# Performance work log

Measured on AMD Instinct MI355X. Metric: run time of the kernel, lower is better.

The kernel has to match this reference:

```python
import jax, jax.numpy as jnp
import numpy as np

FULL_SCALE = 128.0
R = 0.5
TOPK = 4


def setup_inputs() -> dict:
    key = jax.random.key(0)
    k0, k1, k2, k3, k4 = jax.random.split(key, 5)
    B, Na, Nb, D = 16, 2048, 2048, 512
    coords_a = jax.random.randint(k0, (B, Na, 3), 0, 128, dtype=jnp.int32)
    coords_b = jax.random.randint(k1, (B, Nb, 3), 0, 128, dtype=jnp.int32)
    feats_a = jax.random.normal(k2, (B, Na, D), jnp.float32)
    feats_b = jax.random.normal(k3, (B, Nb, D), jnp.float32)
    W = jax.random.normal(k4, (2 * D, D), jnp.float32) / np.sqrt(2 * D).astype(np.float32)
    bias = jnp.zeros((D,), jnp.float32)
    return {"feats_a": feats_a, "feats_b": feats_b, "W": W, "bias": bias,
            "coords_a": coords_a, "coords_b": coords_b}


def _pairwise_l2(ca, cb):
    # ca: [B,Na,3], cb: [B,Nb,3] -> [B,Na,Nb], scaled by full_scale
    x2 = jnp.sum(ca * ca, axis=-1)[:, :, None]
    y2 = jnp.sum(cb * cb, axis=-1)[:, None, :]
    sq = x2 + y2 - 2.0 * jnp.einsum('bnd,bmd->bnm', ca, cb)
    return jnp.sqrt(jnp.clip(sq, 0.0, None)) / FULL_SCALE


def reference(feats_a, feats_b, W, bias, coords_a, coords_b):
    ca = coords_a.astype(jnp.float32)
    cb = coords_b.astype(jnp.float32)
    dist = _pairwise_l2(ca, cb)                       # [B,Na,Nb]
    neg_top, idx = jax.lax.top_k(-dist, TOPK)         # smallest TOPK distances
    dist_w = R - jnp.clip(-neg_top, 0.0, R)           # [B,Na,k]
    # gather neighbor features: [B,Na,k,D]
    b_f = jnp.take_along_axis(feats_b[:, None, :, :], idx[:, :, :, None], axis=2)
    a_f = feats_a[:, :, None, :]                      # broadcast over k
    h = jnp.concatenate([b_f, a_f - b_f], axis=-1)    # [B,Na,k,2D]
    fused = jnp.sum(jax.nn.relu(h @ W + bias) * dist_w[..., None], axis=2)  # [B,Na,D]
    # ME.cat(a, tmp): concatenate features along channel dim
    return jnp.concatenate([feats_a, fused], axis=-1)  # [B,Na,2D]
```

## Files before the change

### kernel.cpp

```cpp
#include <hip/hip_runtime.h>
#include <hip/hip_bf16.h>
#include <cstdint>
#include <cstddef>

#define NA   2048
#define NB   2048
#define DD   512
#define PADK 40

typedef __attribute__((ext_vector_type(8))) short bf16x8;
typedef __attribute__((ext_vector_type(4))) float f32x4;
typedef unsigned short u16;
typedef unsigned int   u32;

__device__ __forceinline__ u16 f2b_hw(float f) {
    u32 w;
    asm("v_cvt_pk_bf16_f32 %0, %1, %2" : "=v"(w) : "v"(f), "v"(f));
    return (u16)w;
}
__device__ __forceinline__ float b2f(u16 h) {
    return __uint_as_float(((u32)h) << 16);
}
__device__ __forceinline__ u32 umin32(u32 a, u32 b) { return a < b ? a : b; }
__device__ __forceinline__ u32 umax32(u32 a, u32 b) { return a > b ? a : b; }
__device__ __forceinline__ u32 med3u(u32 a, u32 b, u32 c) {
    return umax32(umin32(a, b), umin32(umax32(a, b), c));
}

#define GLDS16(gsrc, ldst)                                                  \
    __builtin_amdgcn_global_load_lds(                                       \
        (const __attribute__((address_space(1))) void*)(gsrc),              \
        (__attribute__((address_space(3))) void*)(ldst), 16, 0, 0)

__global__ __launch_bounds__(256) void prep_w(const float* __restrict__ W,
                                              u16* __restrict__ W2T,
                                              u16* __restrict__ WdT) {
    __shared__ float s2[64][65];
    __shared__ float sd[64][65];
    int kb = blockIdx.x * 64, nb = blockIdx.y * 64;
    int tid = threadIdx.x;
    int c = tid & 63, r0 = tid >> 6;
    #pragma unroll
    for (int p = 0; p < 16; ++p) {
        int r = p * 4 + r0;
        float w1 = W[(size_t)(kb + r) * DD + nb + c];
        float w2 = W[(size_t)(512 + kb + r) * DD + nb + c];
        s2[r][c] = w2;
        sd[r][c] = w1 - w2;
    }
    __syncthreads();
    #pragma unroll
    for (int p = 0; p < 16; ++p) {
        int n = p * 4 + r0;
        W2T[(size_t)(nb + n) * DD + kb + c] = f2b_hw(s2[c][n]);
        WdT[(size_t)(nb + n) * DD + kb + c] = f2b_hw(sd[c][n]);
    }
}

__global__ __launch_bounds__(512) void topk_kernel(const int* __restrict__ ca,
                                                   const int* __restrict__ cb,
                                                   int* __restrict__ idx_out,
                                                   float* __restrict__ w_out,
                                                   const float* __restrict__ fa,
                                                   float* __restrict__ out) {
    __shared__ u32 pcb[NB];
    __shared__ u32 part[3 * 128 * 4];
    int b = blockIdx.y;
    int tid = threadIdx.x;
    for (int p = tid; p < NB; p += 512) {
        const int* c = cb + ((size_t)b * NB + p) * 3;
        pcb[p] = (u32)c[0] | ((u32)c[1] << 8) | ((u32)c[2] << 16);
    }
    __syncthreads();

    int q = tid & 127, g = tid >> 7;
    int i = blockIdx.x * 128 + q;
    const int* ac = ca + ((size_t)b * NA + i) * 3;
    int ax = ac[0], ay = ac[1], az = ac[2];

    u32 k0 = ~0u, k1 = ~0u, k2 = ~0u, k3 = ~0u;
    int j0 = g * 512;
    #pragma unroll 8
    for (int jj = 0; jj < 512; ++jj) {
        int j = j0 + jj;
        u32 p = pcb[j];
        int dx = ax - (int)(p & 255u);
        int dy = ay - (int)((p >> 8) & 255u);
        int dz = az - (int)(p >> 16);
        u32 s = (u32)(__mul24(dx, dx) + __mul24(dy, dy) + __mul24(dz, dz));
        u32 key = (s << 11) | (u32)j;
        u32 nk0 = umin32(k0, key);
        u32 nk1 = med3u(key, k0, k1);
        u32 nk2 = med3u(key, k1, k2);
        u32 nk3 = med3u(key, k2, k3);
        k0 = nk0; k1 = nk1; k2 = nk2; k3 = nk3;
    }
    if (g) {
        u32* pp = &part[((g - 1) * 128 + q) * 4];
        pp[0] = k0; pp[1] = k1; pp[2] = k2; pp[3] = k3;
    }
    __syncthreads();
    if (g == 0) {
        #pragma unroll
        for (int L = 0; L < 3; ++L) {
            const u32* pp = &part[(L * 128 + q) * 4];
            #pragma unroll
            for (int t = 0; t < 4; ++t) {
                u32 key = pp[t];
                u32 nk0 = umin32(k0, key);
                u32 nk1 = med3u(key, k0, k1);
                u32 nk2 = med3u(key, k1, k2);
                u32 nk3 = med3u(key, k2, k3);
                k0 = nk0; k1 = nk1; k2 = nk2; k3 = nk3;
            }
        }
        size_t o = ((size_t)b * NA + i) * 4;
        u32 ks[4] = {k0, k1, k2, k3};
        #pragma unroll
        for (int t = 0; t < 4; ++t) {
            idx_out[o + t] = (int)(ks[t] & 2047u);
            float d = sqrtf((float)(ks[t] >> 11)) * (1.0f / 128.0f);
            w_out[o + t] = 0.5f - fminf(d, 0.5f);
        }
    }

    int cid = blockIdx.y * gridDim.x + blockIdx.x;
    const float* src = fa + (size_t)cid * 128 * DD;
    float* dst = out + (size_t)cid * 128 * 1024;
    #pragma unroll 4
    for (int it = 0; it < 32; ++it) {
        int flat = it * 512 + tid;
        int row = flat >> 7;
        int c4  = flat & 127;
        f32x4 v = *(const f32x4*)(src + (size_t)row * DD + c4 * 4);
        *(f32x4*)(dst + (size_t)row * 1024 + c4 * 4) = v;
    }
}

template<bool FUSED>
__global__ __launch_bounds__(256) void gemm_kernel(const float* __restrict__ A,
                                                   const u16* __restrict__ BT,
                                                   u16* __restrict__ C,
                                                   const int* __restrict__ idxb,
                                                   const float* __restrict__ wb,
                                                   const float* __restrict__ bias,
                                                   const u16* __restrict__ Qb,
                                                   float* __restrict__ out) {
    __shared__ __align__(16) char smem[FUSED ? 33792 : 26624];
    float* As = (float*)smem;
    u16*  Bs  = (u16*)(smem + 16384);

    const int tid  = threadIdx.x;
    const int lane = tid & 63;
    const int wave = tid >> 6;
    const int mb   = blockIdx.x;
    const int m0 = (((mb & 7) << 5) | (mb >> 3)) * 128;
    const int n0 = blockIdx.y * 128;
    const int l15 = lane & 15;
    const int lk8 = (lane >> 4) * 8;
    const int qa  = lk8 >> 2;

    const int srow  = lane >> 3;
    const int squad = (lane & 7) ^ srow;

    const int brow = tid >> 2;
    const int bcol = (tid & 3) * 8;

    const int wr = (wave >> 1) * 64;
    const int wc = (wave & 1) * 64;

    f32x4 acc[4][4];
    #pragma unroll
    for (int m = 0; m < 4; ++m)
        #pragma unroll
        for (int n = 0; n < 4; ++n)
            acc[m][n] = (f32x4){0.f, 0.f, 0.f, 0.f};

    int aoff[4][2];
    #pragma unroll
    for (int m = 0; m < 4; ++m) {
        int R = wr + m * 16 + l15;
        int sx = R & 7;
        aoff[m][0] = R * 128 + ((qa ^ sx) << 4);
        aoff[m][1] = R * 128 + (((qa + 1) ^ sx) << 4);
    }
    const char* AsB = (const char*)As;

    const float* asrc[4];
    #pragma unroll
    for (int p = 0; p < 4; ++p)
        asrc[p] = A + (size_t)(m0 + p * 32 + wave * 8 + srow) * DD + squad * 4;
    const u16* bsrc[2];
    #pragma unroll
    for (int p = 0; p < 2; ++p)
        bsrc[p] = BT + (size_t)(n0 + p * 64 + brow) * DD + bcol;

    for (int kk = 0; kk < DD; kk += 32) {
        bf16x8 bv0 = *(const bf16x8*)(bsrc[0] + kk);
        bf16x8 bv1 = *(const bf16x8*)(bsrc[1] + kk);
        #pragma unroll
        for (int p = 0; p < 4; ++p)
            GLDS16(asrc[p] + kk, As + (p * 32 + wave * 8) * 32);
        *(bf16x8*)(&Bs[brow * PADK + bcol]) = bv0;
        *(bf16x8*)(&Bs[(64 + brow) * PADK + bcol]) = bv1;
        __syncthreads();

        bf16x8 af[4], bfr[4];
        #pragma unroll
        for (int m = 0; m < 4; ++m) {
            f32x4 lo = *(const f32x4*)(AsB + aoff[m][0]);
            f32x4 hi = *(const f32x4*)(AsB + aoff[m][1]);
            u32 w0, w1, w2, w3;
            asm("v_cvt_pk_bf16_f32 %0, %1, %2" : "=v"(w0) : "v"(lo[0]), "v"(lo[1]));
            asm("v_cvt_pk_bf16_f32 %0, %1, %2" : "=v"(w1) : "v"(lo[2]), "v"(lo[3]));
            asm("v_cvt_pk_bf16_f32 %0, %1, %2" : "=v"(w2) : "v"(hi[0]), "v"(hi[1]));
            asm("v_cvt_pk_bf16_f32 %0, %1, %2" : "=v"(w3) : "v"(hi[2]), "v"(hi[3]));
            union { u32 u[4]; bf16x8 v; } cv;
            cv.u[0] = w0; cv.u[1] = w1; cv.u[2] = w2; cv.u[3] = w3;
            af[m] = cv.v;
        }
        #pragma unroll
        for (int n = 0; n < 4; ++n)
            bfr[n] = *(const bf16x8*)(&Bs[(wc + n * 16 + l15) * PADK + lk8]);

        #pragma unroll
        for (int m = 0; m < 4; ++m)
            #pragma unroll
            for (int n = 0; n < 4; ++n)
                acc[m][n] = __builtin_amdgcn_mfma_f32_16x16x32_bf16(
                    af[m], bfr[n], acc[m][n], 0, 0, 0);
        __syncthreads();
    }

    const int r4 = (lane >> 4) * 4;

    if (!FUSED) {
        #pragma unroll
        for (int m = 0; m < 4; ++m)
            #pragma unroll
            for (int n = 0; n < 4; ++n)
                #pragma unroll
                for (int j = 0; j < 4; ++j) {
                    int row = m0 + wr + m * 16 + r4 + j;
                    int col = n0 + wc + n * 16 + l15;
                    C[(size_t)row * DD + col] = f2b_hw(acc[m][n][j]);
                }
        return;
    }

    float bi[4];
    #pragma unroll
    for (int n = 0; n < 4; ++n)
        bi[n] = bias[n0 + wc + n * 16 + l15];

    u16* Ps = (u16*)smem;
    #pragma unroll
    for (int m = 0; m < 4; ++m)
        #pragma unroll
        for (int n = 0; n < 4; ++n)
            #pragma unroll
            for (int j = 0; j < 4; ++j)
                Ps[(wr + m * 16 + r4 + j) * 132 + (wc + n * 16 + l15)] =
                    f2b_hw(acc[m][n][j] + bi[n]);
    __syncthreads();

    const int g = tid >> 4, l16 = tid & 15;
    const int bb = m0 >> 11;
    const u16* qs = Qb + ((size_t)bb << 20);
    #pragma unroll
    for (int k = 0; k < 8; ++k) {
        const int r  = g * 8 + k;
        const int gr = m0 + r;
        int4  iv = *(const int4*)(idxb + (size_t)gr * 4);
        f32x4 wv = *(const f32x4*)(wb + (size_t)gr * 4);
        bf16x8 p8 = *(const bf16x8*)(Ps + r * 132 + l16 * 8);
        bf16x8 q0 = *(const bf16x8*)(qs + (size_t)iv.x * DD + n0 + l16 * 8);
        bf16x8 q1 = *(const bf16x8*)(qs + (size_t)iv.y * DD + n0 + l16 * 8);
        bf16x8 q2 = *(const bf16x8*)(qs + (size_t)iv.z * DD + n0 + l16 * 8);
        bf16x8 q3 = *(const bf16x8*)(qs + (size_t)iv.w * DD + n0 + l16 * 8);
        float o[8];
        #pragma unroll
        for (int j = 0; j < 8; ++j) {
            float p = b2f((u16)p8[j]);
            float s;
            s  = fmaxf(p + b2f((u16)q0[j]), 0.f) * wv[0];
            s += fmaxf(p + b2f((u16)q1[j]), 0.f) * wv[1];
            s += fmaxf(p + b2f((u16)q2[j]), 0.f) * wv[2];
            s += fmaxf(p + b2f((u16)q3[j]), 0.f) * wv[3];
            o[j] = s;
        }
        float* op = out + (size_t)gr * 1024 + 512 + n0 + l16 * 8;
        *(f32x4*)op       = (f32x4){o[0], o[1], o[2], o[3]};
        *(f32x4*)(op + 4) = (f32x4){o[4], o[5], o[6], o[7]};
    }
}

extern "C" void kernel_launch(void* const* d_in, const int* in_sizes, int n_in,
                              void* d_out, int out_size, void* d_ws, size_t ws_size,
                              hipStream_t stream) {
    const float* fa   = (const float*)d_in[0];
    const float* fb   = (const float*)d_in[1];
    const float* W    = (const float*)d_in[2];
    const float* bias = (const float*)d_in[3];
    const int*   ca   = (const int*)d_in[4];
    const int*   cb   = (const int*)d_in[5];
    float* out = (float*)d_out;

    char* ws = (char*)d_ws;
    u16*   Qb   = (u16*)(ws);
    u16*   W2T  = (u16*)(ws + 33554432);
    u16*   WdT  = (u16*)(ws + 34078720);
    int*   idxb = (int*)(ws + 34603008);
    float* wb   = (float*)(ws + 35127296);

    dim3 pg(8, 8);
    prep_w<<<pg, 256, 0, stream>>>(W, W2T, WdT);

    dim3 tg(16, 16);
    topk_kernel<<<tg, 512, 0, stream>>>(ca, cb, idxb, wb, fa, out);

    dim3 gg(256, 4);
    gemm_kernel<false><<<gg, 256, 0, stream>>>(fb, WdT, Qb, nullptr, nullptr,
                                               nullptr, nullptr, nullptr);
    gemm_kernel<true><<<gg, 256, 0, stream>>>(fa, W2T, nullptr, idxb, wb,
                                              bias, Qb, out);
}
```

Baseline: 152.5 us.

## Pre-convert feature matrices to bf16 and load both GEMM operands via direct-to-LDS

Adds a separate conversion pass that casts feats_a and feats_b to bf16 buffers in the workspace, and moves the feats_a copy into the output from the topk kernel into that pass. The GEMM kernels then read bf16 A tiles, halving A-operand traffic and LDS footprint. Both A and B are staged with global_load_lds, and the per-iteration fp32-to-bf16 conversion in the GEMM inner loop is removed. The cost is an extra full read and write pass over both feature arrays. The new unpadded, unswizzled LDS layout with a 32-element row stride may cause bank conflicts on fragment reads.

Result: slower. 171.8 us (+12.6%).

```diff
diff --git a/kernel.cpp b/kernel.cpp
--- a/kernel.cpp
+++ b/kernel.cpp
@@ -6,7 +6,6 @@
 #define NA   2048
 #define NB   2048
 #define DD   512
-#define PADK 40
 
 typedef __attribute__((ext_vector_type(8))) short bf16x8;
 typedef __attribute__((ext_vector_type(4))) float f32x4;
@@ -25,6 +24,16 @@
 __device__ __forceinline__ u32 umax32(u32 a, u32 b) { return a > b ? a : b; }
 __device__ __forceinline__ u32 med3u(u32 a, u32 b, u32 c) {
     return umax32(umin32(a, b), umin32(umax32(a, b), c));
+}
+__device__ __forceinline__ bf16x8 cvt8(f32x4 v0, f32x4 v1) {
+    u32 w0, w1, w2, w3;
+    asm("v_cvt_pk_bf16_f32 %0, %1, %2" : "=v"(w0) : "v"(v0[0]), "v"(v0[1]));
+    asm("v_cvt_pk_bf16_f32 %0, %1, %2" : "=v"(w1) : "v"(v0[2]), "v"(v0[3]));
+    asm("v_cvt_pk_bf16_f32 %0, %1, %2" : "=v"(w2) : "v"(v1[0]), "v"(v1[1]));
+    asm("v_cvt_pk_bf16_f32 %0, %1, %2" : "=v"(w3) : "v"(v1[2]), "v"(v1[3]));
+    union { u32 u[4]; bf16x8 v; } cv;
+    cv.u[0] = w0; cv.u[1] = w1; cv.u[2] = w2; cv.u[3] = w3;
+    return cv.v;
 }
 
 #define GLDS16(gsrc, ldst)                                                  \
@@ -57,12 +66,36 @@
     }
 }
 
+__global__ __launch_bounds__(256) void convert_kernel(const float* __restrict__ fa,
+                                                      const float* __restrict__ fb,
+                                                      u16* __restrict__ Ab,
+                                                      u16* __restrict__ Bb,
+                                                      float* __restrict__ out) {
+    const int nthreads = 2048 * 256;
+    int t = blockIdx.x * 256 + threadIdx.x;
+    for (int s = t; s < 32768 * 64; s += nthreads) {
+        int row = s >> 6, c8 = (s & 63) << 3;
+        const float* src = fa + ((size_t)row << 9) + c8;
+        f32x4 v0 = *(const f32x4*)src;
+        f32x4 v1 = *(const f32x4*)(src + 4);
+        float* d = out + ((size_t)row << 10) + c8;
+        *(f32x4*)d = v0;
+        *(f32x4*)(d + 4) = v1;
+        *(bf16x8*)(Ab + ((size_t)row << 9) + c8) = cvt8(v0, v1);
+    }
+    for (int s = t; s < 32768 * 64; s += nthreads) {
+        int row = s >> 6, c8 = (s & 63) << 3;
+        const float* src = fb + ((size_t)row << 9) + c8;
+        f32x4 v0 = *(const f32x4*)src;
+        f32x4 v1 = *(const f32x4*)(src + 4);
+        *(bf16x8*)(Bb + ((size_t)row << 9) + c8) = cvt8(v0, v1);
+    }
+}
+
 __global__ __launch_bounds__(512) void topk_kernel(const int* __restrict__ ca,
                                                    const int* __restrict__ cb,
                                                    int* __restrict__ idx_out,
-                                                   float* __restrict__ w_out,
-                                                   const float* __restrict__ fa,
-                                                   float* __restrict__ out) {
+                                                   float* __restrict__ w_out) {
     __shared__ u32 pcb[NB];
     __shared__ u32 part[3 * 128 * 4];
     int b = blockIdx.y;
@@ -123,22 +156,10 @@
             w_out[o + t] = 0.5f - fminf(d, 0.5f);
         }
     }
-
-    int cid = blockIdx.y * gridDim.x + blockIdx.x;
-    const float* src = fa + (size_t)cid * 128 * DD;
-    float* dst = out + (size_t)cid * 128 * 1024;
-    #pragma unroll 4
-    for (int it = 0; it < 32; ++it) {
-        int flat = it * 512 + tid;
-        int row = flat >> 7;
-        int c4  = flat & 127;
-        f32x4 v = *(const f32x4*)(src + (size_t)row * DD + c4 * 4);
-        *(f32x4*)(dst + (size_t)row * 1024 + c4 * 4) = v;
-    }
 }
 
 template<bool FUSED>
-__global__ __launch_bounds__(256) void gemm_kernel(const float* __restrict__ A,
+__global__ __launch_bounds__(256) void gemm_kernel(const u16* __restrict__ A,
                                                    const u16* __restrict__ BT,
                                                    u16* __restrict__ C,
                                                    const int* __restrict__ idxb,
@@ -146,9 +167,9 @@
                                                    const float* __restrict__ bias,
                                                    const u16* __restrict__ Qb,
                                                    float* __restrict__ out) {
-    __shared__ __align__(16) char smem[FUSED ? 33792 : 26624];
-    float* As = (float*)smem;
-    u16*  Bs  = (u16*)(smem + 16384);
+    __shared__ __align__(16) char smem[FUSED ? 33792 : 16384];
+    u16* As = (u16*)smem;
+    u16* Bs = (u16*)(smem + 8192);
 
     const int tid  = threadIdx.x;
     const int lane = tid & 63;
@@ -158,13 +179,9 @@
     const int n0 = blockIdx.y * 128;
     const int l15 = lane & 15;
     const int lk8 = (lane >> 4) * 8;
-    const int qa  = lk8 >> 2;
-
-    const int srow  = lane >> 3;
-    const int squad = (lane & 7) ^ srow;
-
-    const int brow = tid >> 2;
-    const int bcol = (tid & 3) * 8;
+
+    const int srow = lane >> 2;
+    const int scol = (lane & 3) * 8;
 
     const int wr = (wave >> 1) * 64;
     const int wc = (wave & 1) * 64;
@@ -176,52 +193,29 @@
         for (int n = 0; n < 4; ++n)
             acc[m][n] = (f32x4){0.f, 0.f, 0.f, 0.f};
 
-    int aoff[4][2];
-    #pragma unroll
-    for (int m = 0; m < 4; ++m) {
-        int R = wr + m * 16 + l15;
-        int sx = R & 7;
-        aoff[m][0] = R * 128 + ((qa ^ sx) << 4);
-        aoff[m][1] = R * 128 + (((qa + 1) ^ sx) << 4);
-    }
-    const char* AsB = (const char*)As;
-
-    const float* asrc[4];
-    #pragma unroll
-    for (int p = 0; p < 4; ++p)
-        asrc[p] = A + (size_t)(m0 + p * 32 + wave * 8 + srow) * DD + squad * 4;
+    const u16* asrc[2];
     const u16* bsrc[2];
     #pragma unroll
-    for (int p = 0; p < 2; ++p)
-        bsrc[p] = BT + (size_t)(n0 + p * 64 + brow) * DD + bcol;
+    for (int p = 0; p < 2; ++p) {
+        asrc[p] = A  + (size_t)(m0 + wave * 32 + p * 16 + srow) * DD + scol;
+        bsrc[p] = BT + (size_t)(n0 + wave * 32 + p * 16 + srow) * DD + scol;
+    }
 
     for (int kk = 0; kk < DD; kk += 32) {
-        bf16x8 bv0 = *(const bf16x8*)(bsrc[0] + kk);
-        bf16x8 bv1 = *(const bf16x8*)(bsrc[1] + kk);
-        #pragma unroll
-        for (int p = 0; p < 4; ++p)
-            GLDS16(asrc[p] + kk, As + (p * 32 + wave * 8) * 32);
-        *(bf16x8*)(&Bs[brow * PADK + bcol]) = bv0;
-        *(bf16x8*)(&Bs[(64 + brow) * PADK + bcol]) = bv1;
+        #pragma unroll
+        for (int p = 0; p < 2; ++p) {
+            GLDS16(asrc[p] + kk, As + wave * 1024 + p * 512);
+            GLDS16(bsrc[p] + kk, Bs + wave * 1024 + p * 512);
+        }
         __syncthreads();
 
         bf16x8 af[4], bfr[4];
         #pragma unroll
-        for (int m = 0; m < 4; ++m) {
-            f32x4 lo = *(const f32x4*)(AsB + aoff[m][0]);
-            f32x4 hi = *(const f32x4*)(AsB + aoff[m][1]);
-            u32 w0, w1, w2, w3;
-            asm("v_cvt_pk_bf16_f32 %0, %1, %2" : "=v"(w0) : "v"(lo[0]), "v"(lo[1]));
-            asm("v_cvt_pk_bf16_f32 %0, %1, %2" : "=v"(w1) : "v"(lo[2]), "v"(lo[3]));
-            asm("v_cvt_pk_bf16_f32 %0, %1, %2" : "=v"(w2) : "v"(hi[0]), "v"(hi[1]));
-            asm("v_cvt_pk_bf16_f32 %0, %1, %2" : "=v"(w3) : "v"(hi[2]), "v"(hi[3]));
-            union { u32 u[4]; bf16x8 v; } cv;
-            cv.u[0] = w0; cv.u[1] = w1; cv.u[2] = w2; cv.u[3] = w3;
-            af[m] = cv.v;
-        }
+        for (int m = 0; m < 4; ++m)
+            af[m] = *(const bf16x8*)(&As[(wr + m * 16 + l15) * 32 + lk8]);
         #pragma unroll
         for (int n = 0; n < 4; ++n)
-            bfr[n] = *(const bf16x8*)(&Bs[(wc + n * 16 + l15) * PADK + lk8]);
+            bfr[n] = *(const bf16x8*)(&Bs[(wc + n * 16 + l15) * 32 + lk8]);
 
         #pragma unroll
         for (int m = 0; m < 4; ++m)
@@ -254,6 +248,7 @@
         bi[n] = bias[n0 + wc + n * 16 + l15];
 
     u16* Ps = (u16*)smem;
+    __syncthreads();
     #pragma unroll
     for (int m = 0; m < 4; ++m)
         #pragma unroll
@@ -308,20 +303,24 @@
 
     char* ws = (char*)d_ws;
     u16*   Qb   = (u16*)(ws);
-    u16*   W2T  = (u16*)(ws + 33554432);
-    u16*   WdT  = (u16*)(ws + 34078720);
-    int*   idxb = (int*)(ws + 34603008);
-    float* wb   = (float*)(ws + 35127296);
+    u16*   Ab   = (u16*)(ws + 33554432);
+    u16*   Bb   = (u16*)(ws + 67108864);
+    u16*   W2T  = (u16*)(ws + 100663296);
+    u16*   WdT  = (u16*)(ws + 101187584);
+    int*   idxb = (int*)(ws + 101711872);
+    float* wb   = (float*)(ws + 102236160);
 
     dim3 pg(8, 8);
     prep_w<<<pg, 256, 0, stream>>>(W, W2T, WdT);
 
     dim3 tg(16, 16);
-    topk_kernel<<<tg, 512, 0, stream>>>(ca, cb, idxb, wb, fa, out);
+    topk_kernel<<<tg, 512, 0, stream>>>(ca, cb, idxb, wb);
+
+    convert_kernel<<<2048, 256, 0, stream>>>(fa, fb, Ab, Bb, out);
 
     dim3 gg(256, 4);
-    gemm_kernel<false><<<gg, 256, 0, stream>>>(fb, WdT, Qb, nullptr, nullptr,
+    gemm_kernel<false><<<gg, 256, 0, stream>>>(Bb, WdT, Qb, nullptr, nullptr,
                                                nullptr, nullptr, nullptr);
-    gemm_kernel<true><<<gg, 256, 0, stream>>>(fa, W2T, nullptr, idxb, wb,
+    gemm_kernel<true><<<gg, 256, 0, stream>>>(Ab, W2T, nullptr, idxb, wb,
                                               bias, Qb, out);
 }
```
